# Kernel optimization log

Hardware: AMD Instinct MI355X
Metric: run time of the kernel (lower is better)

Reference implementation:

```python
import jax, jax.numpy as jnp
import numpy as np

N_NODES = 50000
N_EDGES = 1600000
IN_DIM = 6
H = 64


def _sage_conv(x, src, dst, W_l, b_l, W_r, num_nodes):
    """PyG SAGEConv (aggr='mean'): out = lin_l(mean_{j in N(i)} x_j) + lin_r(x_i).
    lin_l has bias, lin_r has no bias (PyG default)."""
    # mean-aggregate neighbor features at destination nodes
    agg = jax.ops.segment_sum(x[src], dst, num_segments=num_nodes)          # [N, d]
    cnt = jax.ops.segment_sum(jnp.ones((src.shape[0],), x.dtype), dst,
                              num_segments=num_nodes)                        # [N]
    mean = agg / jnp.maximum(cnt, 1.0)[:, None]
    return mean @ W_l + b_l + x @ W_r


def setup_inputs() -> dict:
    key = jax.random.key(0)
    ks = jax.random.split(key, 8)
    x = jax.random.normal(ks[0], (N_NODES, IN_DIM), dtype=jnp.float32)
    edge_index = jax.random.randint(ks[1], (2, N_EDGES), 0, N_NODES, dtype=jnp.int64)
    # Kaiming-ish scaled params
    def lin(k, fan_in, fan_out):
        return jax.random.normal(k, (fan_in, fan_out), dtype=jnp.float32) / np.sqrt(fan_in)
    return {
        "x": x,
        "edge_index": edge_index,
        "W1_l": lin(ks[2], IN_DIM, H),
        "b1_l": jnp.zeros((H,), jnp.float32),
        "W1_r": lin(ks[3], IN_DIM, H),
        "W2_l": lin(ks[4], H, H),
        "b2_l": jnp.zeros((H,), jnp.float32),
        "W2_r": lin(ks[5], H, H),
    }


def reference(x, edge_index, W1_l, b1_l, W1_r, W2_l, b2_l, W2_r):
    src, dst = edge_index[0], edge_index[1]
    n = x.shape[0]
    z = jax.nn.relu(_sage_conv(x, src, dst, W1_l, b1_l, W1_r, n))  # [N, H]
    z = _sage_conv(z, src, dst, W2_l, b2_l, W2_r, n)               # [N, H]
    return z
```

## Files before the change

kernel.cpp:

```cpp
#include <hip/hip_runtime.h>

#define N_NODES 50000
#define N_EDGES 1600000
#define IN_DIM 6
#define H 64

#define NBUCKET 196
#define NBLK 196
#define EPB 8192
#define BCAP 9216

#define L2PAD 72
#define ZPLANE ((size_t)(N_NODES + 1) * 32)

__device__ __forceinline__ float bf2f(unsigned short u) {
    return __uint_as_float(((unsigned int)u) << 16);
}
__device__ __forceinline__ unsigned short f2bf(float f) {
    unsigned int u = __float_as_uint(f);
    u += 0x7fffu + ((u >> 16) & 1u);
    return (unsigned short)(u >> 16);
}

__global__ __launch_bounds__(1024) void scatter_bucketed(
        const int* __restrict__ ei,
        const float* __restrict__ x,
        int* __restrict__ gcur,
        unsigned int* __restrict__ ebin,
        const float* __restrict__ W2l,
        const float* __restrict__ W2r,
        unsigned short* __restrict__ Wlt,
        unsigned short* __restrict__ Wrt,
        unsigned short* __restrict__ z,
        float* __restrict__ xp) {
    int t = threadIdx.x;
    int gid = blockIdx.x * 1024 + t;
    if (gid < N_NODES) {
        const float2* xr = (const float2*)(x + (size_t)gid * IN_DIM);
        float2 p0 = xr[0], p1 = xr[1], p2 = xr[2];
        float4* xw = (float4*)(xp + ((size_t)gid << 3));
        xw[0] = make_float4(p0.x, p0.y, p1.x, p1.y);
        xw[1] = make_float4(p2.x, p2.y, 0.f, 0.f);
    }
    if (blockIdx.x == NBLK) {
        for (int i = t; i < H * H; i += 1024) {
            int k = i >> 6, f = i & 63;
            Wlt[f * H + k] = f2bf(W2l[i]);
            Wrt[f * H + k] = f2bf(W2r[i]);
        }
        if (t < 64)
            z[(size_t)(t >> 5) * ZPLANE + (size_t)N_NODES * 32 + (t & 31)] = 0;
        return;
    }
    __shared__ unsigned int sedge[EPB];
    __shared__ int hist[NBUCKET];
    __shared__ int cur[NBUCKET];
    if (t < NBUCKET) hist[t] = 0;
    __syncthreads();
    int e0 = blockIdx.x * EPB;
    int cnt = min(EPB, N_EDGES - e0);
    const int4* s4 = (const int4*)(ei + e0);
    const int4* d4 = (const int4*)(ei + N_EDGES + e0);
    for (int k = t; k * 4 < cnt; k += 1024) {
        int4 sv = s4[k];
        int4 dv = d4[k];
        sedge[k * 4 + 0] = ((unsigned)sv.x << 16) | (unsigned)dv.x;
        sedge[k * 4 + 1] = ((unsigned)sv.y << 16) | (unsigned)dv.y;
        sedge[k * 4 + 2] = ((unsigned)sv.z << 16) | (unsigned)dv.z;
        sedge[k * 4 + 3] = ((unsigned)sv.w << 16) | (unsigned)dv.w;
        atomicAdd(&hist[dv.x >> 8], 1);
        atomicAdd(&hist[dv.y >> 8], 1);
        atomicAdd(&hist[dv.z >> 8], 1);
        atomicAdd(&hist[dv.w >> 8], 1);
    }
    __syncthreads();
    if (t < NBUCKET) cur[t] = atomicAdd(&gcur[t], hist[t]);
    __syncthreads();
    for (int k = t; k * 4 < cnt; k += 1024) {
#pragma unroll
        for (int j = 0; j < 4; j++) {
            unsigned int p = sedge[k * 4 + j];
            int b = (int)(p & 0xffffu) >> 8;
            int pos = atomicAdd(&cur[b], 1);
            if (pos < BCAP) ebin[(size_t)b * BCAP + pos] = p;
        }
    }
}

__global__ __launch_bounds__(1024) void bucket_layer1(
        const unsigned int* __restrict__ ebin,
        const int* __restrict__ gcur,
        const float* __restrict__ xp,
        const float* __restrict__ W1l,
        const float* __restrict__ b1,
        const float* __restrict__ W1r,
        int2* __restrict__ rowpair,
        unsigned short* __restrict__ esrc,
        unsigned short* __restrict__ z) {
    __shared__ int raw[BCAP];
    __shared__ unsigned short ssrc[BCAP];
    __shared__ int sdeg[256];
    __shared__ int sstart[256];
    __shared__ int scur[256];
    __shared__ int wsum[4];
    __shared__ float sW1l[IN_DIM * H];
    __shared__ float sW1r[IN_DIM * H];
    float* smx   = (float*)raw;
    float* spart = (float*)raw + 4096;

    int t = threadIdx.x;
    int lane = t & 63, w = t >> 6;
    int b = blockIdx.x;
    int base = b << 8;
    int nn = min(256, N_NODES - base);
    int ebase = b * BCAP;
    int cnt = min(gcur[b], BCAP);

    if (t < 256) sdeg[t] = 0;
    if (t < IN_DIM * H) { sW1l[t] = W1l[t]; sW1r[t] = W1r[t]; }
    for (int i = t; i < cnt; i += 1024) raw[i] = (int)ebin[ebase + i];
    __syncthreads();
    for (int i = t; i < cnt; i += 1024) atomicAdd(&sdeg[raw[i] & 0xff], 1);
    __syncthreads();
    int v = 0, s = 0;
    if (t < 256) {
        v = sdeg[t]; s = v;
#pragma unroll
        for (int off = 1; off < 64; off <<= 1) {
            int u = __shfl_up(s, off);
            if (lane >= off) s += u;
        }
        if (lane == 63) wsum[w] = s;
    }
    __syncthreads();
    if (t < 256) {
        int woff = 0;
        for (int k = 0; k < w; k++) woff += wsum[k];
        int excl = s - v + woff;
        sstart[t] = excl;
        scur[t] = excl;
        if (t < nn) rowpair[base + t] = make_int2(ebase + excl, ebase + excl + v);
    }
    __syncthreads();
    for (int i = t; i < cnt; i += 1024) {
        int p = raw[i];
        int pos = atomicAdd(&scur[p & 0xff], 1);
        ssrc[pos] = (unsigned short)((unsigned)p >> 16);
    }
    __syncthreads();
    for (int i = t; i < cnt; i += 1024)
        esrc[ebase + i] = ssrc[i];
    for (int i = t; i < nn * 8; i += 1024) {
        int node = i >> 3, k = i & 7;
        if (k < 6) smx[node * 16 + 6 + k] = xp[(size_t)(base + node) * 8 + k];
    }

    int node = t & 255, q = t >> 8;
    float a0 = 0.f, a1 = 0.f, a2 = 0.f, a3 = 0.f, a4 = 0.f, a5 = 0.f;
    int deg = 0, st = 0;
    if (node < nn) { deg = sdeg[node]; st = sstart[node]; }
    int e = st + q, end = st + deg;
    while (e + 12 < end) {
        float4 P[8];
#pragma unroll
        for (int u = 0; u < 4; u++) {
            int src = ssrc[e + u * 4];
            const float4* xs = (const float4*)(xp + ((size_t)src << 3));
            P[2 * u] = xs[0]; P[2 * u + 1] = xs[1];
        }
#pragma unroll
        for (int u = 0; u < 4; u++) {
            a0 += P[2 * u].x; a1 += P[2 * u].y; a2 += P[2 * u].z;
            a3 += P[2 * u].w; a4 += P[2 * u + 1].x; a5 += P[2 * u + 1].y;
        }
        e += 16;
    }
    while (e < end) {
        int src = ssrc[e];
        const float4* xs = (const float4*)(xp + ((size_t)src << 3));
        float4 p0 = xs[0], p1 = xs[1];
        a0 += p0.x; a1 += p0.y; a2 += p0.z;
        a3 += p0.w; a4 += p1.x; a5 += p1.y;
        e += 4;
    }
    if (q > 0 && node < nn) {
        float* sp = &spart[(q - 1) * (256 * 6) + node * 6];
        sp[0] = a0; sp[1] = a1; sp[2] = a2; sp[3] = a3; sp[4] = a4; sp[5] = a5;
    }
    __syncthreads();
    if (q == 0 && node < nn) {
        float inv = 1.0f / fmaxf((float)deg, 1.0f);
        const float* p1p = &spart[0 * (256 * 6) + node * 6];
        const float* p2p = &spart[1 * (256 * 6) + node * 6];
        const float* p3p = &spart[2 * (256 * 6) + node * 6];
        smx[node * 16 + 0] = (a0 + p1p[0] + p2p[0] + p3p[0]) * inv;
        smx[node * 16 + 1] = (a1 + p1p[1] + p2p[1] + p3p[1]) * inv;
        smx[node * 16 + 2] = (a2 + p1p[2] + p2p[2] + p3p[2]) * inv;
        smx[node * 16 + 3] = (a3 + p1p[3] + p2p[3] + p3p[3]) * inv;
        smx[node * 16 + 4] = (a4 + p1p[4] + p2p[4] + p3p[4]) * inv;
        smx[node * 16 + 5] = (a5 + p1p[5] + p2p[5] + p3p[5]) * inv;
    }
    __syncthreads();

    int feat = t & 63, ng = t >> 6;
    float wl[IN_DIM], wr[IN_DIM];
#pragma unroll
    for (int k = 0; k < IN_DIM; k++) { wl[k] = sW1l[k * H + feat]; wr[k] = sW1r[k * H + feat]; }
    float bias = b1[feat];
    int plane = feat >> 5, f5 = feat & 31;
    unsigned short* zw = z + (size_t)plane * ZPLANE + f5;
    for (int nb = ng; nb < nn; nb += 16) {
        const float4* row = (const float4*)&smx[nb * 16];
        float4 r0 = row[0], r1 = row[1], r2 = row[2];
        float acc = bias;
        acc += r0.x * wl[0] + r0.y * wl[1] + r0.z * wl[2]
             + r0.w * wl[3] + r1.x * wl[4] + r1.y * wl[5];
        acc += r1.z * wr[0] + r1.w * wr[1] + r2.x * wr[2]
             + r2.y * wr[3] + r2.z * wr[4] + r2.w * wr[5];
        zw[(size_t)(base + nb) * 32] = f2bf(fmaxf(acc, 0.0f));
    }
}

__global__ __launch_bounds__(512) void layer2_mfma(
        const unsigned short* __restrict__ zin,
        const int2* __restrict__ rowpair,
        const unsigned short* __restrict__ esrc,
        const unsigned short* __restrict__ Wlt,
        const float* __restrict__ b2,
        const unsigned short* __restrict__ Wrt,
        float* __restrict__ out) {
    typedef short bf16x8 __attribute__((ext_vector_type(8)));
    typedef float f32x4 __attribute__((ext_vector_type(4)));
    __shared__ __attribute__((aligned(16))) unsigned short smean[32 * L2PAD];
    __shared__ __attribute__((aligned(16))) unsigned short szl[32 * L2PAD];
    __shared__ __attribute__((aligned(16))) unsigned short sWl[64 * L2PAD];
    __shared__ __attribute__((aligned(16))) unsigned short sWr[64 * L2PAD];

    int t = threadIdx.x;
    int w = t >> 6, lane = t & 63;
    int g8 = lane >> 3, l8 = lane & 7;
    int n0 = blockIdx.x * 32;

    {
        const ushort4* wl4 = (const ushort4*)Wlt;
        const ushort4* wr4 = (const ushort4*)Wrt;
        for (int qi = t; qi < H * H / 4; qi += 512) {
            int f = qi >> 4, kq = qi & 15;
            *(ushort4*)&sWl[f * L2PAD + kq * 4] = wl4[qi];
            *(ushort4*)&sWr[f * L2PAD + kq * 4] = wr4[qi];
        }
    }

#pragma unroll 1
    for (int pass = 0; pass < 2; pass++) {
        const unsigned short* zp = zin + (size_t)pass * ZPLANE;
        for (int q = 0; q < 4; q++) {
            int ln = w * 4 + q;
            int n = n0 + ln;
            bool valid = (n < N_NODES);
            int r0 = 0, r1 = 0;
            if (valid) { int2 rp = rowpair[n]; r0 = rp.x; r1 = rp.y; }
            float4 acc = make_float4(0.f, 0.f, 0.f, 0.f);
            for (int base = r0; base < r1; base += 64) {
                int ii = base + lane;
                int idx = (ii < r1) ? (int)esrc[ii] : N_NODES;
                int rem = r1 - base;
#pragma unroll
                for (int tt = 0; tt < 4; tt++) {
                    int s = __shfl(idx, tt * 8 + g8);
                    const ushort4* zr = (const ushort4*)(zp + (size_t)s * 32);
                    ushort4 vv = zr[l8];
                    acc.x += bf2f(vv.x); acc.y += bf2f(vv.y);
                    acc.z += bf2f(vv.z); acc.w += bf2f(vv.w);
                }
                if (rem > 32) {
#pragma unroll
                    for (int tt = 4; tt < 8; tt++) {
                        int s = __shfl(idx, tt * 8 + g8);
                        const ushort4* zr = (const ushort4*)(zp + (size_t)s * 32);
                        ushort4 vv = zr[l8];
                        acc.x += bf2f(vv.x); acc.y += bf2f(vv.y);
                        acc.z += bf2f(vv.z); acc.w += bf2f(vv.w);
                    }
                }
            }
#pragma unroll
            for (int off = 8; off < 64; off <<= 1) {
                acc.x += __shfl_xor(acc.x, off);
                acc.y += __shfl_xor(acc.y, off);
                acc.z += __shfl_xor(acc.z, off);
                acc.w += __shfl_xor(acc.w, off);
            }
            float inv = 1.0f / fmaxf((float)(r1 - r0), 1.0f);
            if (g8 == 0) {
                ushort4 mb;
                mb.x = f2bf(acc.x * inv); mb.y = f2bf(acc.y * inv);
                mb.z = f2bf(acc.z * inv); mb.w = f2bf(acc.w * inv);
                *(ushort4*)&smean[ln * L2PAD + pass * 32 + l8 * 4] = mb;
            }
            if (pass == 0) {
                int nz = valid ? n : N_NODES;
                szl[ln * L2PAD + lane] =
                    zin[(size_t)(lane >> 5) * ZPLANE + (size_t)nz * 32 + (lane & 31)];
            }
        }
    }
    __syncthreads();

    int g = lane >> 4, lg = lane & 15;
    int nb = w >> 2, fb = w & 3;
    f32x4 acc = {0.f, 0.f, 0.f, 0.f};
#pragma unroll
    for (int ks = 0; ks < 2; ks++) {
        int ko = ks * 32 + g * 8;
        bf16x8 aM = *(const bf16x8*)&smean[(nb * 16 + lg) * L2PAD + ko];
        bf16x8 aZ = *(const bf16x8*)&szl[(nb * 16 + lg) * L2PAD + ko];
        bf16x8 bL = *(const bf16x8*)&sWl[(fb * 16 + lg) * L2PAD + ko];
        bf16x8 bR = *(const bf16x8*)&sWr[(fb * 16 + lg) * L2PAD + ko];
        acc = __builtin_amdgcn_mfma_f32_16x16x32_bf16(aM, bL, acc, 0, 0, 0);
        acc = __builtin_amdgcn_mfma_f32_16x16x32_bf16(aZ, bR, acc, 0, 0, 0);
    }
    float bias = b2[fb * 16 + lg];
#pragma unroll
    for (int r = 0; r < 4; r++) {
        int node = n0 + nb * 16 + g * 4 + r;
        if (node < N_NODES)
            out[(size_t)node * H + fb * 16 + lg] = acc[r] + bias;
    }
}

extern "C" void kernel_launch(void* const* d_in, const int* in_sizes, int n_in,
                              void* d_out, int out_size, void* d_ws, size_t ws_size,
                              hipStream_t stream) {
    const float* x   = (const float*)d_in[0];
    const int*   ei  = (const int*)d_in[1];
    const float* W1l = (const float*)d_in[2];
    const float* b1  = (const float*)d_in[3];
    const float* W1r = (const float*)d_in[4];
    const float* W2l = (const float*)d_in[5];
    const float* b2  = (const float*)d_in[6];
    const float* W2r = (const float*)d_in[7];
    float* out = (float*)d_out;

    int* gcur = (int*)d_ws;
    int2* rowpair = (int2*)(gcur + 208);
    unsigned int*   ebin = (unsigned int*)(rowpair + N_NODES);
    unsigned short* esrc = (unsigned short*)(ebin + (size_t)NBUCKET * BCAP);
    unsigned short* z    = esrc + (size_t)NBUCKET * BCAP;
    unsigned short* Wlt  = z + 2 * ZPLANE;
    unsigned short* Wrt  = Wlt + H * H;
    float* xp = (float*)(Wrt + H * H);

    hipMemsetAsync(gcur, 0, NBUCKET * sizeof(int), stream);

    scatter_bucketed<<<NBLK + 1, 1024, 0, stream>>>(ei, x, gcur, ebin,
                                                    W2l, W2r, Wlt, Wrt, z, xp);
    bucket_layer1<<<NBUCKET, 1024, 0, stream>>>(ebin, gcur, xp, W1l, b1, W1r,
                                                rowpair, esrc, z);
    layer2_mfma<<<(N_NODES + 31) / 32, 512, 0, stream>>>(z, rowpair, esrc,
                                                         Wlt, b2, Wrt, out);
}
```

Baseline: 154.8 us.

## Software-pipeline neighbor gathers across nodes in layer-2 aggregation kernel

Prefetches the row ranges and the first 64 edge indices for all four nodes of each wave up front. Gathers are double-buffered, so one node's 64 neighbor rows are in flight while the previous node's are accumulated. Nodes with more than 64 edges fall back to a loop. This targets gather latency that the serial per-node loop exposed, at the cost of more registers and unconditional loads of padding rows for short neighbor lists.

```diff
diff --git a/kernel.cpp b/kernel.cpp
--- a/kernel.cpp
+++ b/kernel.cpp
@@ -240,6 +240,17 @@
     int w = t >> 6, lane = t & 63;
     int g8 = lane >> 3, l8 = lane & 7;
     int n0 = blockIdx.x * 32;
+    int ln0 = w * 4;
+
+    int r0a[4], r1a[4], idxv[4];
+#pragma unroll
+    for (int j = 0; j < 4; j++) {
+        int n = n0 + ln0 + j;
+        int2 rp = (n < N_NODES) ? rowpair[n] : make_int2(0, 0);
+        r0a[j] = rp.x; r1a[j] = rp.y;
+        int ii = rp.x + lane;
+        idxv[j] = (ii < rp.y) ? (int)esrc[ii] : N_NODES;
+    }
 
     {
         const ushort4* wl4 = (const ushort4*)Wlt;
@@ -251,59 +262,86 @@
         }
     }
 
+#define ISSUE(J, V)                                                        \
+    {                                                                      \
+        int idx_ = idxv[J];                                                \
+        _Pragma("unroll")                                                  \
+        for (int tt = 0; tt < 8; tt++) {                                   \
+            int s_ = __shfl(idx_, tt * 8 + g8);                            \
+            V[tt] = *(const ushort4*)(zp + (size_t)s_ * 32 + l8 * 4);      \
+        }                                                                  \
+    }
+#define ACCUM(V, AC)                                                       \
+    {                                                                      \
+        _Pragma("unroll")                                                  \
+        for (int tt = 0; tt < 8; tt++) {                                   \
+            AC.x += bf2f(V[tt].x); AC.y += bf2f(V[tt].y);                  \
+            AC.z += bf2f(V[tt].z); AC.w += bf2f(V[tt].w);                  \
+        }                                                                  \
+    }
+#define FALLBACK(J, AC)                                                    \
+    if (r1a[J] - r0a[J] > 64) {                                            \
+        for (int eb = r0a[J] + 64; eb < r1a[J]; eb += 64) {                \
+            int ii2 = eb + lane;                                           \
+            int idx2 = (ii2 < r1a[J]) ? (int)esrc[ii2] : N_NODES;          \
+            int rem = r1a[J] - eb;                                         \
+            _Pragma("unroll")                                              \
+            for (int tt = 0; tt < 8; tt++) {                               \
+                if (tt * 8 >= rem) break;                \
+                int s_ = __shfl(idx2, tt * 8 + g8);                        \
+                ushort4 vv = *(const ushort4*)(zp + (size_t)s_ * 32 + l8 * 4); \
+                AC.x += bf2f(vv.x); AC.y += bf2f(vv.y);                    \
+                AC.z += bf2f(vv.z); AC.w += bf2f(vv.w);                    \
+            }                                                              \
+        }                                                                  \
+    }
+#define REDUCE(J, AC)                                                      \
+    {                                                                      \
+        _Pragma("unroll")                                                  \
+        for (int off = 8; off < 64; off <<= 1) {                           \
+            AC.x += __shfl_xor(AC.x, off);                                 \
+            AC.y += __shfl_xor(AC.y, off);                                 \
+            AC.z += __shfl_xor(AC.z, off);                                 \
+            AC.w += __shfl_xor(AC.w, off);                                 \
+        }                                                                  \
+        float inv_ = 1.0f / fmaxf((float)(r1a[J] - r0a[J]), 1.0f);         \
+        if (g8 == 0) {                                                     \
+            ushort4 mb;                                                    \
+            mb.x = f2bf(AC.x * inv_); mb.y = f2bf(AC.y * inv_);            \
+            mb.z = f2bf(AC.z * inv_); mb.w = f2bf(AC.w * inv_);            \
+            *(ushort4*)&smean[(ln0 + J) * L2PAD + pass * 32 + l8 * 4] = mb; \
+        }                                                                  \
+    }
+
 #pragma unroll 1
     for (int pass = 0; pass < 2; pass++) {
         const unsigned short* zp = zin + (size_t)pass * ZPLANE;
-        for (int q = 0; q < 4; q++) {
-            int ln = w * 4 + q;
-            int n = n0 + ln;
-            bool valid = (n < N_NODES);
-            int r0 = 0, r1 = 0;
-            if (valid) { int2 rp = rowpair[n]; r0 = rp.x; r1 = rp.y; }
-            float4 acc = make_float4(0.f, 0.f, 0.f, 0.f);
-            for (int base = r0; base < r1; base += 64) {
-                int ii = base + lane;
-                int idx = (ii < r1) ? (int)esrc[ii] : N_NODES;
-                int rem = r1 - base;
-#pragma unroll
-                for (int tt = 0; tt < 4; tt++) {
-                    int s = __shfl(idx, tt * 8 + g8);
-                    const ushort4* zr = (const ushort4*)(zp + (size_t)s * 32);
-                    ushort4 vv = zr[l8];
-                    acc.x += bf2f(vv.x); acc.y += bf2f(vv.y);
-                    acc.z += bf2f(vv.z); acc.w += bf2f(vv.w);
-                }
-                if (rem > 32) {
-#pragma unroll
-                    for (int tt = 4; tt < 8; tt++) {
-                        int s = __shfl(idx, tt * 8 + g8);
-                        const ushort4* zr = (const ushort4*)(zp + (size_t)s * 32);
-                        ushort4 vv = zr[l8];
-                        acc.x += bf2f(vv.x); acc.y += bf2f(vv.y);
-                        acc.z += bf2f(vv.z); acc.w += bf2f(vv.w);
-                    }
-                }
-            }
-#pragma unroll
-            for (int off = 8; off < 64; off <<= 1) {
-                acc.x += __shfl_xor(acc.x, off);
-                acc.y += __shfl_xor(acc.y, off);
-                acc.z += __shfl_xor(acc.z, off);
-                acc.w += __shfl_xor(acc.w, off);
-            }
-            float inv = 1.0f / fmaxf((float)(r1 - r0), 1.0f);
-            if (g8 == 0) {
-                ushort4 mb;
-                mb.x = f2bf(acc.x * inv); mb.y = f2bf(acc.y * inv);
-                mb.z = f2bf(acc.z * inv); mb.w = f2bf(acc.w * inv);
-                *(ushort4*)&smean[ln * L2PAD + pass * 32 + l8 * 4] = mb;
-            }
-            if (pass == 0) {
-                int nz = valid ? n : N_NODES;
-                szl[ln * L2PAD + lane] =
-                    zin[(size_t)(lane >> 5) * ZPLANE + (size_t)nz * 32 + (lane & 31)];
-            }
-        }
+        ushort4 vA[8], vB[8];
+        float4 ac;
+        ISSUE(0, vA)
+        ISSUE(1, vB)
+        ac = make_float4(0.f, 0.f, 0.f, 0.f);
+        ACCUM(vA, ac) FALLBACK(0, ac) REDUCE(0, ac)
+        ISSUE(2, vA)
+        ac = make_float4(0.f, 0.f, 0.f, 0.f);
+        ACCUM(vB, ac) FALLBACK(1, ac) REDUCE(1, ac)
+        ISSUE(3, vB)
+        ac = make_float4(0.f, 0.f, 0.f, 0.f);
+        ACCUM(vA, ac) FALLBACK(2, ac) REDUCE(2, ac)
+        ac = make_float4(0.f, 0.f, 0.f, 0.f);
+        ACCUM(vB, ac) FALLBACK(3, ac) REDUCE(3, ac)
+    }
+#undef ISSUE
+#undef ACCUM
+#undef FALLBACK
+#undef REDUCE
+
+#pragma unroll
+    for (int j = 0; j < 4; j++) {
+        int n = n0 + ln0 + j;
+        int nz = (n < N_NODES) ? n : N_NODES;
+        szl[(ln0 + j) * L2PAD + lane] =
+            zin[(size_t)(lane >> 5) * ZPLANE + (size_t)nz * 32 + (lane & 31)];
     }
     __syncthreads();
 
```

Result: slower. 161.6 us (+4.4%).
